# Kernel optimization log

Measured on AMD Instinct MI355X. Metric: run time of the kernel, lower is better.

The kernel has to match this reference:

```python
import jax, jax.numpy as jnp
import numpy as np

D_MODEL = 1024
D_STATE = 64
D_CONV = 4
EXPAND = 2
HEADDIM = 128
D_INNER = EXPAND * D_MODEL          # 2048
NHEADS = D_INNER // HEADDIM         # 16
CONV_DIM = D_INNER + 2 * D_STATE    # 2176 (ngroups=1)
D_IN_PROJ = 2 * D_INNER + 2 * D_STATE + NHEADS  # 4240
EPS = 1e-5


def _silu(x):
    return x * jax.nn.sigmoid(x)


def _causal_conv_silu(x, w, b):
    # x: [b, l, c]; w: [c, k] depthwise; b: [c]. Causal: pad left k-1, keep first L.
    L = x.shape[1]
    xp = jnp.pad(x, ((0, 0), (D_CONV - 1, 0), (0, 0)))
    out = b
    for k in range(D_CONV):  # tiny fixed kernel loop
        out = out + xp[:, k:k + L, :] * w[:, k]
    return _silu(out)


def _ssd_scan(x, dt, A, B, C):
    # x: [b,l,h,p], dt: [b,l,h], A: [h], B,C: [b,l,n] (ngroups=1, shared over heads)
    bsz = x.shape[0]

    def step(h, inp):
        x_t, dt_t, B_t, C_t = inp           # [b,h,p], [b,h], [b,n], [b,n]
        dA = jnp.exp(dt_t * A)              # [b,h]
        h = h * dA[:, :, None, None] + jnp.einsum('bh,bhp,bn->bhpn', dt_t, x_t, B_t)
        y = jnp.einsum('bhpn,bn->bhp', h, C_t)
        return h, y

    h0 = jnp.zeros((bsz, NHEADS, HEADDIM, D_STATE), x.dtype)
    xs = (jnp.moveaxis(x, 1, 0), jnp.moveaxis(dt, 1, 0),
          jnp.moveaxis(B, 1, 0), jnp.moveaxis(C, 1, 0))
    _, y = jax.lax.scan(step, h0, xs)       # y: [l,b,h,p]
    return jnp.moveaxis(y, 0, 1)


def _branch(zxbcdt, conv_w, conv_b, dt_bias, A_log, D, norm_w):
    # One direction of bimamba-v2: split, conv+silu, selective scan, D skip, gated RMSNorm.
    b, l, _ = zxbcdt.shape
    z = zxbcdt[..., :D_INNER]
    xBC = zxbcdt[..., D_INNER:D_INNER + CONV_DIM]
    dt = jax.nn.softplus(zxbcdt[..., -NHEADS:] + dt_bias)  # [b,l,h]
    A = -jnp.exp(A_log)                                     # [h]
    xBC = _causal_conv_silu(xBC, conv_w, conv_b)
    x = xBC[..., :D_INNER].reshape(b, l, NHEADS, HEADDIM)
    Bm = xBC[..., D_INNER:D_INNER + D_STATE]
    Cm = xBC[..., D_INNER + D_STATE:]
    y = _ssd_scan(x, dt, A, Bm, Cm) + D[None, None, :, None] * x
    y = y.reshape(b, l, D_INNER)
    # RMSNormGated, norm_before_gate=False: gate first, then normalize
    yz = y * _silu(z)
    return yz * jax.lax.rsqrt(jnp.mean(yz * yz, axis=-1, keepdims=True) + EPS) * norm_w


def setup_inputs() -> dict:
    key = jax.random.key(0)
    ks = jax.random.split(key, 12)
    B, L = 2, 4096

    def gauss(k, shape, scale):
        return jax.random.normal(k, shape, jnp.float32) * scale

    def dt_bias_init(k):
        lo, hi = np.log(0.001), np.log(0.1)
        dt = jnp.exp(jax.random.uniform(k, (NHEADS,)) * (hi - lo) + lo)
        dt = jnp.clip(dt, 1e-4, None)
        return dt + jnp.log(-jnp.expm1(-dt))  # softplus-inverse of dt

    return {
        'u': jax.random.normal(ks[0], (B, L, D_MODEL), jnp.float32),
        'in_proj_w': gauss(ks[1], (D_IN_PROJ, D_MODEL), 0.02),
        'conv_w': gauss(ks[2], (CONV_DIM, D_CONV), 0.2),
        'conv_b': jnp.zeros((CONV_DIM,), jnp.float32),
        'conv_w_bw': gauss(ks[3], (CONV_DIM, D_CONV), 0.2),
        'conv_b_bw': jnp.zeros((CONV_DIM,), jnp.float32),
        'dt_bias': dt_bias_init(ks[4]),
        'dt_bias_bw': dt_bias_init(ks[5]),
        'A_log': jnp.log(jax.random.uniform(ks[6], (NHEADS,), minval=1.0, maxval=16.0)),
        'A_b_log': jnp.log(jax.random.uniform(ks[7], (NHEADS,), minval=1.0, maxval=16.0)),
        'D': jnp.ones((NHEADS,), jnp.float32),
        'D_b': jnp.ones((NHEADS,), jnp.float32),
        'norm_w': jnp.ones((D_INNER,), jnp.float32),
        'out_proj_w': gauss(ks[8], (D_MODEL, D_INNER), 0.02),
    }


def reference(u, in_proj_w, conv_w, conv_b, conv_w_bw, conv_b_bw, dt_bias, dt_bias_bw,
              A_log, A_b_log, D, D_b, norm_w, out_proj_w):
    zxbcdt = u @ in_proj_w.T                                   # [b,l,4240]
    y_fw = _branch(zxbcdt, conv_w, conv_b, dt_bias, A_log, D, norm_w)
    y_bw = _branch(zxbcdt[:, ::-1, :], conv_w_bw, conv_b_bw, dt_bias_bw, A_b_log, D_b, norm_w)
    return (y_fw + y_bw[:, ::-1, :]) @ out_proj_w.T            # divide_out=False
```

## Files before the change

kernel.cpp:

```cpp
#include <hip/hip_runtime.h>
#include <hip/hip_bf16.h>
#include <math.h>

#define BB 2
#define LL 4096
#define DM 1024
#define DIP 4240
#define DIPP 4352
#define DI 2048
#define NH 16
#define HD 128
#define DS 64
#define CDIM 2176
#define MROWS (BB*LL)
#define Q 64
#define NC (LL/Q)
#define BH (BB*NH)
#define STR 72
#define CCH 16
#define NCHK (LL/CCH)

typedef __attribute__((ext_vector_type(8))) short bf16x8;
typedef __attribute__((ext_vector_type(4))) float f32x4;

__device__ __forceinline__ float silu_f(float x) { return x / (1.f + expf(-x)); }
__device__ __forceinline__ float softplus_f(float x) {
    return fmaxf(x, 0.f) + log1pf(expf(-fabsf(x)));
}
__device__ __forceinline__ float bf2f(unsigned short u) {
    return __uint_as_float(((unsigned int)u) << 16);
}
__device__ __forceinline__ unsigned short f2bf(float f) {
    unsigned int x = __float_as_uint(f);
    return (unsigned short)((x + 0x7fff + ((x >> 16) & 1)) >> 16);
}
__device__ __forceinline__ void gll16(const void* g, void* l) {
    __builtin_amdgcn_global_load_lds(
        (const __attribute__((address_space(1))) void*)g,
        (__attribute__((address_space(3))) void*)l,
        16, 0, 0);
}

__global__ __launch_bounds__(256)
void cvt_pad(const float* __restrict__ in, unsigned short* __restrict__ out,
             int rows_real, int rows_pad, int cols)
{
    int idx = blockIdx.x * 256 + threadIdx.x;
    int cols4 = cols >> 2;
    int total = rows_pad * cols4;
    if (idx >= total) return;
    int row = idx / cols4;
    int c4 = (idx - row * cols4) * 4;
    ushort4 o;
    if (row < rows_real) {
        float4 v = *reinterpret_cast<const float4*>(&in[(size_t)row * cols + c4]);
        o.x = f2bf(v.x); o.y = f2bf(v.y); o.z = f2bf(v.z); o.w = f2bf(v.w);
    } else {
        o = make_ushort4(0, 0, 0, 0);
    }
    *reinterpret_cast<ushort4*>(&out[(size_t)row * cols + c4]) = o;
}

__global__ __launch_bounds__(256)
void ucvt(const float* __restrict__ u, unsigned short* __restrict__ ub)
{
    int idx = blockIdx.x * 256 + threadIdx.x;
    const float* src = u + (size_t)idx * 8;
    float4 a = *reinterpret_cast<const float4*>(src);
    float4 b = *reinterpret_cast<const float4*>(src + 4);
    unsigned short o[8];
    o[0] = f2bf(a.x); o[1] = f2bf(a.y); o[2] = f2bf(a.z); o[3] = f2bf(a.w);
    o[4] = f2bf(b.x); o[5] = f2bf(b.y); o[6] = f2bf(b.z); o[7] = f2bf(b.w);
    *reinterpret_cast<uint4*>(&ub[(size_t)idx * 8]) = *reinterpret_cast<const uint4*>(o);
}

template<int OMODE>
__global__ __launch_bounds__(256)
void gemm_mfma(const unsigned short* __restrict__ Ap, int lda,
               const unsigned short* __restrict__ Bp, int K,
               void* __restrict__ Cp, int ldc, int Nreal)
{
    __shared__ alignas(16) unsigned short As[128 * 32];
    __shared__ alignas(16) unsigned short Bs[128 * 32];

    const int t = threadIdx.x;
    const int l = t & 63;
    const int bm = blockIdx.y * 128, bn = blockIdx.x * 128;
    const int wm = ((t >> 6) >> 1) * 64, wn = ((t >> 6) & 1) * 64;

    f32x4 acc[4][4];
    #pragma unroll
    for (int i = 0; i < 4; i++)
        #pragma unroll
        for (int j = 0; j < 4; j++)
            acc[i][j] = (f32x4){0.f, 0.f, 0.f, 0.f};

    for (int k0 = 0; k0 < K; k0 += 32) {
        #pragma unroll
        for (int i = 0; i < 2; i++) {
            int c = i * 256 + t;
            int row = c >> 2, ke = (c & 3) * 8;
            gll16(Ap + (size_t)(bm + row) * lda + k0 + ke, (char*)&As[0] + c * 16);
        }
        #pragma unroll
        for (int i = 0; i < 2; i++) {
            int c = i * 256 + t;
            int row = c >> 2, ke = (c & 3) * 8;
            gll16(Bp + (size_t)(bn + row) * K + k0 + ke, (char*)&Bs[0] + c * 16);
        }
        __syncthreads();

        bf16x8 af[4], bfr[4];
        #pragma unroll
        for (int mi = 0; mi < 4; mi++)
            af[mi] = *reinterpret_cast<const bf16x8*>(
                &As[(wm + mi * 16 + (l & 15)) * 32 + (l >> 4) * 8]);
        #pragma unroll
        for (int nj = 0; nj < 4; nj++)
            bfr[nj] = *reinterpret_cast<const bf16x8*>(
                &Bs[(wn + nj * 16 + (l & 15)) * 32 + (l >> 4) * 8]);
        #pragma unroll
        for (int mi = 0; mi < 4; mi++)
            #pragma unroll
            for (int nj = 0; nj < 4; nj++)
                acc[mi][nj] = __builtin_amdgcn_mfma_f32_16x16x32_bf16(
                    af[mi], bfr[nj], acc[mi][nj], 0, 0, 0);
        __syncthreads();
    }

    const int col_l = l & 15, rgrp = (l >> 4) * 4;
    #pragma unroll
    for (int mi = 0; mi < 4; mi++) {
        #pragma unroll
        for (int r = 0; r < 4; r++) {
            int gm = bm + wm + mi * 16 + rgrp + r;
            #pragma unroll
            for (int nj = 0; nj < 4; nj++) {
                int gn = bn + wn + nj * 16 + col_l;
                float v = acc[mi][nj][r];
                if (OMODE == 0) {
                    if (gn < Nreal)
                        ((unsigned short*)Cp)[(size_t)gm * ldc + gn] = f2bf(v);
                } else {
                    ((float*)Cp)[(size_t)gm * ldc + gn] = v;
                }
            }
        }
    }
}

__global__ __launch_bounds__(256)
void conv_fused(const unsigned short* __restrict__ zx,
                const float* __restrict__ cw0, const float* __restrict__ cb0,
                const float* __restrict__ cw1, const float* __restrict__ cb1,
                unsigned short* __restrict__ x0, unsigned short* __restrict__ x1)
{
    int idx = blockIdx.x * 256 + threadIdx.x;
    int c8 = idx % (CDIM / 8);
    int cg = idx / (CDIM / 8);
    int b  = cg >> 8;
    int ci = cg & (NCHK - 1);
    int c  = c8 * 8;
    int s0 = ci * CCH;

    float wt0[4][8], wt1[4][8], bv0[8], bv1[8];
    #pragma unroll
    for (int ch = 0; ch < 8; ch++) {
        float4 q0 = *reinterpret_cast<const float4*>(&cw0[(c + ch) * 4]);
        float4 q1 = *reinterpret_cast<const float4*>(&cw1[(c + ch) * 4]);
        wt0[0][ch] = q0.x; wt0[1][ch] = q0.y; wt0[2][ch] = q0.z; wt0[3][ch] = q0.w;
        wt1[0][ch] = q1.x; wt1[1][ch] = q1.y; wt1[2][ch] = q1.z; wt1[3][ch] = q1.w;
    }
    {
        float4 a0 = *reinterpret_cast<const float4*>(&cb0[c]);
        float4 a1 = *reinterpret_cast<const float4*>(&cb0[c + 4]);
        bv0[0]=a0.x; bv0[1]=a0.y; bv0[2]=a0.z; bv0[3]=a0.w;
        bv0[4]=a1.x; bv0[5]=a1.y; bv0[6]=a1.z; bv0[7]=a1.w;
        float4 d0 = *reinterpret_cast<const float4*>(&cb1[c]);
        float4 d1 = *reinterpret_cast<const float4*>(&cb1[c + 4]);
        bv1[0]=d0.x; bv1[1]=d0.y; bv1[2]=d0.z; bv1[3]=d0.w;
        bv1[4]=d1.x; bv1[5]=d1.y; bv1[6]=d1.z; bv1[7]=d1.w;
    }

    float win[4][8];

    #define LDROW(SL, S) do {                                                  \
        if ((S) >= 0) {                                                        \
            const unsigned short* _src = &zx[((size_t)b * LL + (S)) * DIP + DI + c]; \
            ushort4 _v0 = *reinterpret_cast<const ushort4*>(_src);             \
            ushort4 _v1 = *reinterpret_cast<const ushort4*>(_src + 4);         \
            win[SL][0] = bf2f(_v0.x); win[SL][1] = bf2f(_v0.y);                \
            win[SL][2] = bf2f(_v0.z); win[SL][3] = bf2f(_v0.w);                \
            win[SL][4] = bf2f(_v1.x); win[SL][5] = bf2f(_v1.y);                \
            win[SL][6] = bf2f(_v1.z); win[SL][7] = bf2f(_v1.w);                \
        } else {                                                               \
            _Pragma("unroll")                                                  \
            for (int _e = 0; _e < 8; _e++) win[SL][_e] = 0.f;                  \
        }                                                                      \
    } while (0)

    #define ZROW(SL) do {                                                      \
        _Pragma("unroll")                                                      \
        for (int _e = 0; _e < 8; _e++) win[SL][_e] = 0.f;                      \
    } while (0)

    #define EMIT0(PH, S) do {                                                  \
        float _a[8]; unsigned short _o[8];                                     \
        _Pragma("unroll")                                                      \
        for (int _ch = 0; _ch < 8; _ch++) {                                    \
            _a[_ch] = bv0[_ch];                                                \
            _a[_ch] = fmaf(wt0[0][_ch], win[((PH)+1)&3][_ch], _a[_ch]);        \
            _a[_ch] = fmaf(wt0[1][_ch], win[((PH)+2)&3][_ch], _a[_ch]);        \
            _a[_ch] = fmaf(wt0[2][_ch], win[((PH)+3)&3][_ch], _a[_ch]);        \
            _a[_ch] = fmaf(wt0[3][_ch], win[(PH)&3][_ch], _a[_ch]);            \
            _o[_ch] = f2bf(silu_f(_a[_ch]));                                   \
        }                                                                      \
        *reinterpret_cast<uint4*>(&x0[((size_t)b * LL + (S)) * CDIM + c]) =    \
            *reinterpret_cast<const uint4*>(_o);                               \
    } while (0)

    #define EMIT1(PH, S) do {                                                  \
        float _a[8]; unsigned short _o[8];                                     \
        _Pragma("unroll")                                                      \
        for (int _ch = 0; _ch < 8; _ch++) {                                    \
            _a[_ch] = bv1[_ch];                                                \
            _a[_ch] = fmaf(wt1[0][_ch], win[(PH)&3][_ch], _a[_ch]);            \
            _a[_ch] = fmaf(wt1[1][_ch], win[((PH)+3)&3][_ch], _a[_ch]);        \
            _a[_ch] = fmaf(wt1[2][_ch], win[((PH)+2)&3][_ch], _a[_ch]);        \
            _a[_ch] = fmaf(wt1[3][_ch], win[((PH)+1)&3][_ch], _a[_ch]);        \
            _o[_ch] = f2bf(silu_f(_a[_ch]));                                   \
        }                                                                      \
        *reinterpret_cast<uint4*>(&x1[((size_t)b * LL + (LL + 2 - (S))) * CDIM + c]) = \
            *reinterpret_cast<const uint4*>(_o);                               \
    } while (0)

    LDROW(1, s0 - 3);
    LDROW(2, s0 - 2);
    LDROW(3, s0 - 1);

    for (int it = 0; it < CCH; it += 4) {
        int sb = s0 + it;
        #pragma unroll
        for (int ph = 0; ph < 4; ph++) {
            int s = sb + ph;
            switch (ph) {
            case 0: LDROW(0, s); EMIT0(0, s); if (s >= 3) EMIT1(0, s); break;
            case 1: LDROW(1, s); EMIT0(1, s); if (s >= 3) EMIT1(1, s); break;
            case 2: LDROW(2, s); EMIT0(2, s); if (s >= 3) EMIT1(2, s); break;
            default: LDROW(3, s); EMIT0(3, s); if (s >= 3) EMIT1(3, s); break;
            }
        }
    }
    if (ci == NCHK - 1) {
        ZROW(0); EMIT1(0, LL);
        ZROW(1); EMIT1(1, LL + 1);
        ZROW(2); EMIT1(2, LL + 2);
    }
    #undef LDROW
    #undef ZROW
    #undef EMIT0
    #undef EMIT1
}

__global__ __launch_bounds__(256)
void ssd_state(const unsigned short* __restrict__ xc, const unsigned short* __restrict__ zx,
               const float* __restrict__ dtb, const float* __restrict__ A_log,
               unsigned short* __restrict__ hbuf, float* __restrict__ dtsum, int dir)
{
    int bh = blockIdx.x / NC;
    int c  = blockIdx.x % NC;
    int b = bh >> 4, h = bh & 15;
    float Ah = -expf(A_log[h]);
    float dtbh = dtb[h];
    int row0 = b * LL + c * Q;

    __shared__ alignas(16) unsigned short XT[128 * STR];
    __shared__ alignas(16) unsigned short wBT[64 * STR];
    __shared__ float dts_s[Q];
    __shared__ float cum_s[Q];

    const int tid = threadIdx.x;
    const int l = tid & 63;
    const int wid = tid >> 6;

    #pragma unroll
    for (int it = 0; it < 4; it++) {
        int idx = it * 256 + tid;
        int j = idx >> 4;
        int pblk = idx & 15;
        const unsigned short* src = &xc[(size_t)(row0 + j) * CDIM + h * HD + pblk * 8];
        ushort4 v0 = *reinterpret_cast<const ushort4*>(src);
        ushort4 v1 = *reinterpret_cast<const ushort4*>(src + 4);
        unsigned short xv[8] = {v0.x, v0.y, v0.z, v0.w, v1.x, v1.y, v1.z, v1.w};
        int jx = j ^ ((pblk & 7) << 3);
        #pragma unroll
        for (int e = 0; e < 8; e++)
            XT[(pblk * 8 + e) * STR + jx] = xv[e];
    }
    if (tid < Q) {
        int rr = c * Q + tid;
        int ls = dir ? (LL - 1 - rr) : rr;
        dts_s[tid] = softplus_f(bf2f(zx[(size_t)(b * LL + ls) * DIP + (DIP - NH) + h]) + dtbh);
    }
    __syncthreads();
    if (tid < Q) {
        float s = 0.f;
        for (int k = 0; k <= tid; k++) s += dts_s[k];
        cum_s[tid] = s;
    }
    __syncthreads();
    float cumlast = cum_s[Q - 1];
    if (tid == 0) dtsum[bh * NC + c] = cumlast;

    #pragma unroll
    for (int it = 0; it < 2; it++) {
        int idx = it * 256 + tid;
        int j = idx >> 3, n0 = (idx & 7) * 8;
        const unsigned short* src = &xc[(size_t)(row0 + j) * CDIM + DI + n0];
        ushort4 v0 = *reinterpret_cast<const ushort4*>(src);
        ushort4 v1 = *reinterpret_cast<const ushort4*>(src + 4);
        unsigned short bv[8] = {v0.x, v0.y, v0.z, v0.w, v1.x, v1.y, v1.z, v1.w};
        float wj = expf(Ah * (cumlast - cum_s[j])) * dts_s[j];
        #pragma unroll
        for (int e = 0; e < 8; e++)
            wBT[(n0 + e) * STR + j] = f2bf(wj * bf2f(bv[e]));
    }
    __syncthreads();

    f32x4 acc[2][4];
    #pragma unroll
    for (int i = 0; i < 2; i++)
        #pragma unroll
        for (int j = 0; j < 4; j++)
            acc[i][j] = (f32x4){0.f, 0.f, 0.f, 0.f};

    const int p0w = wid * 32;
    #pragma unroll
    for (int kk = 0; kk < 2; kk++) {
        bf16x8 af[2], bfr[4];
        #pragma unroll
        for (int mi = 0; mi < 2; mi++) {
            int p = p0w + mi * 16 + (l & 15);
            int col = (kk * 32 + (l >> 4) * 8) ^ (((p >> 3) & 7) << 3);
            af[mi] = *reinterpret_cast<const bf16x8*>(&XT[p * STR + col]);
        }
        #pragma unroll
        for (int nj = 0; nj < 4; nj++)
            bfr[nj] = *reinterpret_cast<const bf16x8*>(
                &wBT[(nj * 16 + (l & 15)) * STR + kk * 32 + (l >> 4) * 8]);
        #pragma unroll
        for (int mi = 0; mi < 2; mi++)
            #pragma unroll
            for (int nj = 0; nj < 4; nj++)
                acc[mi][nj] = __builtin_amdgcn_mfma_f32_16x16x32_bf16(
                    af[mi], bfr[nj], acc[mi][nj], 0, 0, 0);
    }

    size_t hb = ((size_t)c * BH + bh) * (HD * DS);
    #pragma unroll
    for (int mi = 0; mi < 2; mi++)
        #pragma unroll
        for (int r = 0; r < 4; r++) {
            int p = p0w + mi * 16 + (l >> 4) * 4 + r;
            #pragma unroll
            for (int nj = 0; nj < 4; nj++) {
                int n = nj * 16 + (l & 15);
                hbuf[hb + (size_t)p * DS + n] = f2bf(acc[mi][nj][r]);
            }
        }
}

__global__ __launch_bounds__(256)
void ssd_interchunk(unsigned short* __restrict__ hbuf, const float* __restrict__ dtsum,
                    const float* __restrict__ A_log)
{
    int bh  = blockIdx.x >> 5;
    int seg = blockIdx.x & 31;
    int h = bh & 15;
    float Ah = -expf(A_log[h]);
    int off = seg * 256 + threadIdx.x;
    float hst = 0.f;
    for (int c = 0; c < NC; c++) {
        size_t idx = ((size_t)c * BH + bh) * (HD * DS) + off;
        float s = bf2f(hbuf[idx]);
        hbuf[idx] = f2bf(hst);
        hst = fmaf(hst, expf(Ah * dtsum[bh * NC + c]), s);
    }
}

__global__ __launch_bounds__(256)
void ssd_intra(unsigned short* __restrict__ xc, const unsigned short* __restrict__ hbuf,
               const unsigned short* __restrict__ zx, const float* __restrict__ dtb,
               const float* __restrict__ A_log, const float* __restrict__ Dv, int dir)
{
    int bh = blockIdx.x / NC;
    int c  = blockIdx.x % NC;
    int b = bh >> 4, h = bh & 15;
    float Ah = -expf(A_log[h]);
    float Dh = Dv[h];
    float dtbh = dtb[h];
    int row0 = b * LL + c * Q;

    __shared__ alignas(16) unsigned short Cm[64 * STR];
    __shared__ alignas(16) unsigned short Bm[64 * STR];
    __shared__ alignas(16) unsigned short Mw[64 * STR];
    __shared__ alignas(16) unsigned short XT[128 * STR];
    __shared__ alignas(16) unsigned short hm[128 * STR];
    __shared__ float dts_s[Q];
    __shared__ float cum_s[Q];

    const int tid = threadIdx.x;
    const int l = tid & 63;
    const int wid = tid >> 6;

    #pragma unroll
    for (int it = 0; it < 4; it++) {
        int idx = it * 256 + tid;
        int j = idx >> 4;
        int pblk = idx & 15;
        const unsigned short* src = &xc[(size_t)(row0 + j) * CDIM + h * HD + pblk * 8];
        ushort4 v0 = *reinterpret_cast<const ushort4*>(src);
        ushort4 v1 = *reinterpret_cast<const ushort4*>(src + 4);
        unsigned short xv[8] = {v0.x, v0.y, v0.z, v0.w, v1.x, v1.y, v1.z, v1.w};
        int jx = j ^ ((pblk & 7) << 3);
        #pragma unroll
        for (int e = 0; e < 8; e++)
            XT[(pblk * 8 + e) * STR + jx] = xv[e];
    }
    #pragma unroll
    for (int it = 0; it < 2; it++) {
        int idx = it * 256 + tid;
        int j = idx >> 3, n0 = (idx & 7) * 8;
        *reinterpret_cast<uint4*>(&Bm[j * STR + n0]) =
            *reinterpret_cast<const uint4*>(&xc[(size_t)(row0 + j) * CDIM + DI + n0]);
        *reinterpret_cast<uint4*>(&Cm[j * STR + n0]) =
            *reinterpret_cast<const uint4*>(&xc[(size_t)(row0 + j) * CDIM + DI + DS + n0]);
    }
    {
        size_t hb = ((size_t)c * BH + bh) * (HD * DS);
        #pragma unroll
        for (int it = 0; it < 4; it++) {
            int idx = it * 256 + tid;
            int p = idx >> 3, n0 = (idx & 7) * 8;
            *reinterpret_cast<uint4*>(&hm[p * STR + n0]) =
                *reinterpret_cast<const uint4*>(&hbuf[hb + (size_t)p * DS + n0]);
        }
    }
    if (tid < Q) {
        int rr = c * Q + tid;
        int ls = dir ? (LL - 1 - rr) : rr;
        dts_s[tid] = softplus_f(bf2f(zx[(size_t)(b * LL + ls) * DIP + (DIP - NH) + h]) + dtbh);
    }
    __syncthreads();
    if (tid < Q) {
        float s = 0.f;
        for (int k = 0; k <= tid; k++) s += dts_s[k];
        cum_s[tid] = s;
    }
    __syncthreads();

    {
        const int i0 = (wid >> 1) * 32, j0 = (wid & 1) * 32;
        f32x4 g[2][2];
        #pragma unroll
        for (int i = 0; i < 2; i++)
            #pragma unroll
            for (int j = 0; j < 2; j++)
                g[i][j] = (f32x4){0.f, 0.f, 0.f, 0.f};
        #pragma unroll
        for (int kk = 0; kk < 2; kk++) {
            bf16x8 ca[2], bb[2];
            #pragma unroll
            for (int mi = 0; mi < 2; mi++)
                ca[mi] = *reinterpret_cast<const bf16x8*>(
                    &Cm[(i0 + mi * 16 + (l & 15)) * STR + kk * 32 + (l >> 4) * 8]);
            #pragma unroll
            for (int nj = 0; nj < 2; nj++)
                bb[nj] = *reinterpret_cast<const bf16x8*>(
                    &Bm[(j0 + nj * 16 + (l & 15)) * STR + kk * 32 + (l >> 4) * 8]);
            #pragma unroll
            for (int mi = 0; mi < 2; mi++)
                #pragma unroll
                for (int nj = 0; nj < 2; nj++)
                    g[mi][nj] = __builtin_amdgcn_mfma_f32_16x16x32_bf16(
                        ca[mi], bb[nj], g[mi][nj], 0, 0, 0);
        }
        #pragma unroll
        for (int mi = 0; mi < 2; mi++)
            #pragma unroll
            for (int nj = 0; nj < 2; nj++)
                #pragma unroll
                for (int r = 0; r < 4; r++) {
                    int i = i0 + mi * 16 + (l >> 4) * 4 + r;
                    int j = j0 + nj * 16 + (l & 15);
                    float wgt = 0.f;
                    if (j < i)       wgt = expf(Ah * (cum_s[i] - cum_s[j])) * dts_s[j];
                    else if (j == i) wgt = dts_s[j];
                    float mv = g[mi][nj][r] * wgt + (j == i ? Dh : 0.f);
                    Mw[i * STR + j] = f2bf(mv);
                }
    }
    __syncthreads();

    const int yi0 = (wid >> 1) * 32, yp0 = (wid & 1) * 64;
    f32x4 y1[2][4], y2[2][4];
    #pragma unroll
    for (int i = 0; i < 2; i++)
        #pragma unroll
        for (int j = 0; j < 4; j++) {
            y1[i][j] = (f32x4){0.f, 0.f, 0.f, 0.f};
            y2[i][j] = (f32x4){0.f, 0.f, 0.f, 0.f};
        }
    #pragma unroll
    for (int kk = 0; kk < 2; kk++) {
        bf16x8 ma[2], xb[4];
        #pragma unroll
        for (int mi = 0; mi < 2; mi++)
            ma[mi] = *reinterpret_cast<const bf16x8*>(
                &Mw[(yi0 + mi * 16 + (l & 15)) * STR + kk * 32 + (l >> 4) * 8]);
        #pragma unroll
        for (int nj = 0; nj < 4; nj++) {
            int p = yp0 + nj * 16 + (l & 15);
            int col = (kk * 32 + (l >> 4) * 8) ^ (((p >> 3) & 7) << 3);
            xb[nj] = *reinterpret_cast<const bf16x8*>(&XT[p * STR + col]);
        }
        #pragma unroll
        for (int mi = 0; mi < 2; mi++)
            #pragma unroll
            for (int nj = 0; nj < 4; nj++)
                y1[mi][nj] = __builtin_amdgcn_mfma_f32_16x16x32_bf16(
                    ma[mi], xb[nj], y1[mi][nj], 0, 0, 0);
    }
    #pragma unroll
    for (int kk = 0; kk < 2; kk++) {
        bf16x8 ca[2], hbf[4];
        #pragma unroll
        for (int mi = 0; mi < 2; mi++)
            ca[mi] = *reinterpret_cast<const bf16x8*>(
                &Cm[(yi0 + mi * 16 + (l & 15)) * STR + kk * 32 + (l >> 4) * 8]);
        #pragma unroll
        for (int nj = 0; nj < 4; nj++)
            hbf[nj] = *reinterpret_cast<const bf16x8*>(
                &hm[(yp0 + nj * 16 + (l & 15)) * STR + kk * 32 + (l >> 4) * 8]);
        #pragma unroll
        for (int mi = 0; mi < 2; mi++)
            #pragma unroll
            for (int nj = 0; nj < 4; nj++)
                y2[mi][nj] = __builtin_amdgcn_mfma_f32_16x16x32_bf16(
                    ca[mi], hbf[nj], y2[mi][nj], 0, 0, 0);
    }
    __syncthreads();

    unsigned short* Yl = &XT[0];
    #pragma unroll
    for (int mi = 0; mi < 2; mi++)
        #pragma unroll
        for (int r = 0; r < 4; r++) {
            int i = yi0 + mi * 16 + (l >> 4) * 4 + r;
            float Pi = expf(Ah * cum_s[i]);
            #pragma unroll
            for (int nj = 0; nj < 4; nj++) {
                int p = yp0 + nj * 16 + (l & 15);
                Yl[i * 136 + p] = f2bf(y1[mi][nj][r] + Pi * y2[mi][nj][r]);
            }
        }
    __syncthreads();
    #pragma unroll
    for (int it = 0; it < 4; it++) {
        int idx = it * 256 + tid;
        int i = idx >> 4, p0 = (idx & 15) * 8;
        *reinterpret_cast<uint4*>(&xc[(size_t)(row0 + i) * CDIM + h * HD + p0]) =
            *reinterpret_cast<const uint4*>(&Yl[i * 136 + p0]);
    }
}

__global__ __launch_bounds__(256)
void branch_final(const unsigned short* __restrict__ xcin, const unsigned short* __restrict__ zx,
                  const float* __restrict__ nw, unsigned short* __restrict__ xout, int dir)
{
    int row = blockIdx.x;
    int rr = row & (LL - 1);
    int b  = row >> 12;
    int l  = dir ? (LL - 1 - rr) : rr;

    const unsigned short* yrow = xcin + (size_t)row * CDIM;
    const unsigned short* zrow = zx + (size_t)(b * LL + l) * DIP;
    int c = threadIdx.x * 8;

    float v[8];
    float ss = 0.f;
    {
        ushort4 y0 = *reinterpret_cast<const ushort4*>(&yrow[c]);
        ushort4 y1 = *reinterpret_cast<const ushort4*>(&yrow[c + 4]);
        ushort4 z0 = *reinterpret_cast<const ushort4*>(&zrow[c]);
        ushort4 z1 = *reinterpret_cast<const ushort4*>(&zrow[c + 4]);
        unsigned short yv[8] = {y0.x, y0.y, y0.z, y0.w, y1.x, y1.y, y1.z, y1.w};
        unsigned short zv[8] = {z0.x, z0.y, z0.z, z0.w, z1.x, z1.y, z1.z, z1.w};
        #pragma unroll
        for (int ch = 0; ch < 8; ch++) {
            float val = bf2f(yv[ch]) * silu_f(bf2f(zv[ch]));
            v[ch] = val;
            ss = fmaf(val, val, ss);
        }
    }
    #pragma unroll
    for (int o = 32; o > 0; o >>= 1) ss += __shfl_down(ss, o);
    __shared__ float red[4];
    if ((threadIdx.x & 63) == 0) red[threadIdx.x >> 6] = ss;
    __syncthreads();
    ss = red[0] + red[1] + red[2] + red[3];
    float scale = rsqrtf(ss * (1.f / DI) + 1e-5f);

    float w[8];
    {
        float4 w0 = *reinterpret_cast<const float4*>(&nw[c]);
        float4 w1 = *reinterpret_cast<const float4*>(&nw[c + 4]);
        w[0] = w0.x; w[1] = w0.y; w[2] = w0.z; w[3] = w0.w;
        w[4] = w1.x; w[5] = w1.y; w[6] = w1.z; w[7] = w1.w;
    }

    unsigned short* orow = xout + (size_t)(b * LL + l) * CDIM;
    unsigned short o[8];
    if (dir) {
        ushort4 p0 = *reinterpret_cast<const ushort4*>(&orow[c]);
        ushort4 p1 = *reinterpret_cast<const ushort4*>(&orow[c + 4]);
        unsigned short pv[8] = {p0.x, p0.y, p0.z, p0.w, p1.x, p1.y, p1.z, p1.w};
        #pragma unroll
        for (int ch = 0; ch < 8; ch++)
            o[ch] = f2bf(bf2f(pv[ch]) + v[ch] * scale * w[ch]);
    } else {
        #pragma unroll
        for (int ch = 0; ch < 8; ch++)
            o[ch] = f2bf(v[ch] * scale * w[ch]);
    }
    *reinterpret_cast<uint4*>(&orow[c]) = *reinterpret_cast<const uint4*>(o);
}

extern "C" void kernel_launch(void* const* d_in, const int* in_sizes, int n_in,
                              void* d_out, int out_size, void* d_ws, size_t ws_size,
                              hipStream_t stream)
{
    const float* u       = (const float*)d_in[0];
    const float* w_in    = (const float*)d_in[1];
    const float* conv_w  = (const float*)d_in[2];
    const float* conv_b  = (const float*)d_in[3];
    const float* conv_wb = (const float*)d_in[4];
    const float* conv_bb = (const float*)d_in[5];
    const float* dt_bias  = (const float*)d_in[6];
    const float* dt_biasb = (const float*)d_in[7];
    const float* A_log   = (const float*)d_in[8];
    const float* A_b_log = (const float*)d_in[9];
    const float* Dp      = (const float*)d_in[10];
    const float* D_b     = (const float*)d_in[11];
    const float* norm_w  = (const float*)d_in[12];
    const float* w_out   = (const float*)d_in[13];
    float* out = (float*)d_out;

    unsigned short* zx    = (unsigned short*)d_ws;
    unsigned short* xc    = zx + (size_t)MROWS * DIP;
    unsigned short* xc2   = xc + (size_t)MROWS * CDIM;
    unsigned short* hb_ub = xc2 + (size_t)MROWS * CDIM;
    unsigned short* wbin  = hb_ub + (size_t)NC * BH * HD * DS;
    unsigned short* wbout = wbin + (size_t)DIPP * DM;
    float* dtsum = (float*)(wbout + (size_t)DM * DI);

    unsigned short* ub   = hb_ub;
    unsigned short* hbuf = hb_ub;

    cvt_pad<<<(DIPP * (DM / 4) + 255) / 256, 256, 0, stream>>>(w_in, wbin, DIP, DIPP, DM);
    cvt_pad<<<(DM * (DI / 4) + 255) / 256, 256, 0, stream>>>(w_out, wbout, DM, DM, DI);
    ucvt<<<(MROWS * DM / 8) / 256, 256, 0, stream>>>(u, ub);

    {
        dim3 grid(DIPP / 128, MROWS / 128);
        gemm_mfma<0><<<grid, 256, 0, stream>>>(ub, DM, wbin, DM, zx, DIP, DIP);
    }

    conv_fused<<<(CDIM / 8) * BB * NCHK / 256, 256, 0, stream>>>(
        zx, conv_w, conv_b, conv_wb, conv_bb, xc, xc2);

    for (int dir = 0; dir < 2; dir++) {
        const float* dtb = dir ? dt_biasb : dt_bias;
        const float* Al  = dir ? A_b_log  : A_log;
        const float* Dd  = dir ? D_b      : Dp;
        unsigned short* xb = dir ? xc2 : xc;

        ssd_state<<<BH * NC, 256, 0, stream>>>(xb, zx, dtb, Al, hbuf, dtsum, dir);
        ssd_interchunk<<<BH * 32, 256, 0, stream>>>(hbuf, dtsum, Al);
        ssd_intra<<<BH * NC, 256, 0, stream>>>(xb, hbuf, zx, dtb, Al, Dd, dir);
        branch_final<<<MROWS, 256, 0, stream>>>(xb, zx, norm_w, xc, dir);
    }

    {
        dim3 grid(DM / 128, MROWS / 128);
        gemm_mfma<1><<<grid, 256, 0, stream>>>(xc, CDIM, wbout, DI, out, DM, DM);
    }
}
```

Baseline: 513.3 us.

## Fuse both branch finals, swizzle GEMM tiles, shuffle-scan cumsum, coalesce state stores

```diff
diff --git a/kernel.cpp b/kernel.cpp
--- a/kernel.cpp
+++ b/kernel.cpp
@@ -85,7 +85,13 @@
 
     const int t = threadIdx.x;
     const int l = t & 63;
-    const int bm = blockIdx.y * 128, bn = blockIdx.x * 128;
+
+    int lin = blockIdx.y * gridDim.x + blockIdx.x;
+    int nwg = gridDim.x * gridDim.y;
+    int swz = (lin & 7) * (nwg >> 3) + (lin >> 3);
+    int bxs = swz % gridDim.x, bys = swz / gridDim.x;
+
+    const int bm = bys * 128, bn = bxs * 128;
     const int wm = ((t >> 6) >> 1) * 64, wn = ((t >> 6) & 1) * 64;
 
     f32x4 acc[4][4];
@@ -300,13 +306,15 @@
     if (tid < Q) {
         int rr = c * Q + tid;
         int ls = dir ? (LL - 1 - rr) : rr;
-        dts_s[tid] = softplus_f(bf2f(zx[(size_t)(b * LL + ls) * DIP + (DIP - NH) + h]) + dtbh);
-    }
-    __syncthreads();
-    if (tid < Q) {
-        float s = 0.f;
-        for (int k = 0; k <= tid; k++) s += dts_s[k];
-        cum_s[tid] = s;
+        float dtv = softplus_f(bf2f(zx[(size_t)(b * LL + ls) * DIP + (DIP - NH) + h]) + dtbh);
+        float ps = dtv;
+        #pragma unroll
+        for (int o = 1; o < 64; o <<= 1) {
+            float t2 = __shfl_up(ps, o);
+            if (tid >= o) ps += t2;
+        }
+        dts_s[tid] = dtv;
+        cum_s[tid] = ps;
     }
     __syncthreads();
     float cumlast = cum_s[Q - 1];
@@ -356,7 +364,8 @@
                     af[mi], bfr[nj], acc[mi][nj], 0, 0, 0);
     }
 
-    size_t hb = ((size_t)c * BH + bh) * (HD * DS);
+    __syncthreads();
+    unsigned short* Sl = &XT[0];
     #pragma unroll
     for (int mi = 0; mi < 2; mi++)
         #pragma unroll
@@ -365,9 +374,18 @@
             #pragma unroll
             for (int nj = 0; nj < 4; nj++) {
                 int n = nj * 16 + (l & 15);
-                hbuf[hb + (size_t)p * DS + n] = f2bf(acc[mi][nj][r]);
+                Sl[p * STR + n] = f2bf(acc[mi][nj][r]);
             }
         }
+    __syncthreads();
+    size_t hb = ((size_t)c * BH + bh) * (HD * DS);
+    #pragma unroll
+    for (int it = 0; it < 4; it++) {
+        int idx = it * 256 + tid;
+        int p = idx >> 3, n0 = (idx & 7) * 8;
+        *reinterpret_cast<uint4*>(&hbuf[hb + (size_t)p * DS + n0]) =
+            *reinterpret_cast<const uint4*>(&Sl[p * STR + n0]);
+    }
 }
 
 __global__ __launch_bounds__(256)
@@ -449,13 +467,15 @@
     if (tid < Q) {
         int rr = c * Q + tid;
         int ls = dir ? (LL - 1 - rr) : rr;
-        dts_s[tid] = softplus_f(bf2f(zx[(size_t)(b * LL + ls) * DIP + (DIP - NH) + h]) + dtbh);
-    }
-    __syncthreads();
-    if (tid < Q) {
-        float s = 0.f;
-        for (int k = 0; k <= tid; k++) s += dts_s[k];
-        cum_s[tid] = s;
+        float dtv = softplus_f(bf2f(zx[(size_t)(b * LL + ls) * DIP + (DIP - NH) + h]) + dtbh);
+        float ps = dtv;
+        #pragma unroll
+        for (int o = 1; o < 64; o <<= 1) {
+            float t2 = __shfl_up(ps, o);
+            if (tid >= o) ps += t2;
+        }
+        dts_s[tid] = dtv;
+        cum_s[tid] = ps;
     }
     __syncthreads();
 
@@ -575,41 +595,55 @@
 }
 
 __global__ __launch_bounds__(256)
-void branch_final(const unsigned short* __restrict__ xcin, const unsigned short* __restrict__ zx,
-                  const float* __restrict__ nw, unsigned short* __restrict__ xout, int dir)
+void branch_final2(unsigned short* __restrict__ xc_fw, const unsigned short* __restrict__ xc_bw,
+                   const unsigned short* __restrict__ zx, const float* __restrict__ nw)
 {
     int row = blockIdx.x;
-    int rr = row & (LL - 1);
+    int ll = row & (LL - 1);
     int b  = row >> 12;
-    int l  = dir ? (LL - 1 - rr) : rr;
-
-    const unsigned short* yrow = xcin + (size_t)row * CDIM;
-    const unsigned short* zrow = zx + (size_t)(b * LL + l) * DIP;
+
+    unsigned short* yfw = xc_fw + (size_t)row * CDIM;
+    const unsigned short* ybw = xc_bw + ((size_t)b * LL + (LL - 1 - ll)) * CDIM;
+    const unsigned short* zrow = zx + (size_t)row * DIP;
     int c = threadIdx.x * 8;
 
-    float v[8];
-    float ss = 0.f;
+    float vf[8], vb[8];
+    float sf = 0.f, sb = 0.f;
     {
-        ushort4 y0 = *reinterpret_cast<const ushort4*>(&yrow[c]);
-        ushort4 y1 = *reinterpret_cast<const ushort4*>(&yrow[c + 4]);
+        ushort4 f0 = *reinterpret_cast<const ushort4*>(&yfw[c]);
+        ushort4 f1 = *reinterpret_cast<const ushort4*>(&yfw[c + 4]);
+        ushort4 w0 = *reinterpret_cast<const ushort4*>(&ybw[c]);
+        ushort4 w1 = *reinterpret_cast<const ushort4*>(&ybw[c + 4]);
         ushort4 z0 = *reinterpret_cast<const ushort4*>(&zrow[c]);
         ushort4 z1 = *reinterpret_cast<const ushort4*>(&zrow[c + 4]);
-        unsigned short yv[8] = {y0.x, y0.y, y0.z, y0.w, y1.x, y1.y, y1.z, y1.w};
+        unsigned short fv[8] = {f0.x, f0.y, f0.z, f0.w, f1.x, f1.y, f1.z, f1.w};
+        unsigned short wv[8] = {w0.x, w0.y, w0.z, w0.w, w1.x, w1.y, w1.z, w1.w};
         unsigned short zv[8] = {z0.x, z0.y, z0.z, z0.w, z1.x, z1.y, z1.z, z1.w};
         #pragma unroll
         for (int ch = 0; ch < 8; ch++) {
-            float val = bf2f(yv[ch]) * silu_f(bf2f(zv[ch]));
-            v[ch] = val;
-            ss = fmaf(val, val, ss);
-        }
-    }
-    #pragma unroll
-    for (int o = 32; o > 0; o >>= 1) ss += __shfl_down(ss, o);
-    __shared__ float red[4];
-    if ((threadIdx.x & 63) == 0) red[threadIdx.x >> 6] = ss;
-    __syncthreads();
-    ss = red[0] + red[1] + red[2] + red[3];
-    float scale = rsqrtf(ss * (1.f / DI) + 1e-5f);
+            float g = silu_f(bf2f(zv[ch]));
+            float a = bf2f(fv[ch]) * g;
+            float d = bf2f(wv[ch]) * g;
+            vf[ch] = a; vb[ch] = d;
+            sf = fmaf(a, a, sf);
+            sb = fmaf(d, d, sb);
+        }
+    }
+    #pragma unroll
+    for (int o = 32; o > 0; o >>= 1) {
+        sf += __shfl_down(sf, o);
+        sb += __shfl_down(sb, o);
+    }
+    __shared__ float redf[4], redb[4];
+    if ((threadIdx.x & 63) == 0) {
+        redf[threadIdx.x >> 6] = sf;
+        redb[threadIdx.x >> 6] = sb;
+    }
+    __syncthreads();
+    sf = redf[0] + redf[1] + redf[2] + redf[3];
+    sb = redb[0] + redb[1] + redb[2] + redb[3];
+    float scf = rsqrtf(sf * (1.f / DI) + 1e-5f);
+    float scb = rsqrtf(sb * (1.f / DI) + 1e-5f);
 
     float w[8];
     {
@@ -618,22 +652,11 @@
         w[0] = w0.x; w[1] = w0.y; w[2] = w0.z; w[3] = w0.w;
         w[4] = w1.x; w[5] = w1.y; w[6] = w1.z; w[7] = w1.w;
     }
-
-    unsigned short* orow = xout + (size_t)(b * LL + l) * CDIM;
     unsigned short o[8];
-    if (dir) {
-        ushort4 p0 = *reinterpret_cast<const ushort4*>(&orow[c]);
-        ushort4 p1 = *reinterpret_cast<const ushort4*>(&orow[c + 4]);
-        unsigned short pv[8] = {p0.x, p0.y, p0.z, p0.w, p1.x, p1.y, p1.z, p1.w};
-        #pragma unroll
-        for (int ch = 0; ch < 8; ch++)
-            o[ch] = f2bf(bf2f(pv[ch]) + v[ch] * scale * w[ch]);
-    } else {
-        #pragma unroll
-        for (int ch = 0; ch < 8; ch++)
-            o[ch] = f2bf(v[ch] * scale * w[ch]);
-    }
-    *reinterpret_cast<uint4*>(&orow[c]) = *reinterpret_cast<const uint4*>(o);
+    #pragma unroll
+    for (int ch = 0; ch < 8; ch++)
+        o[ch] = f2bf((vf[ch] * scf + vb[ch] * scb) * w[ch]);
+    *reinterpret_cast<uint4*>(&yfw[c]) = *reinterpret_cast<const uint4*>(o);
 }
 
 extern "C" void kernel_launch(void* const* d_in, const int* in_sizes, int n_in,
@@ -688,8 +711,8 @@
         ssd_state<<<BH * NC, 256, 0, stream>>>(xb, zx, dtb, Al, hbuf, dtsum, dir);
         ssd_interchunk<<<BH * 32, 256, 0, stream>>>(hbuf, dtsum, Al);
         ssd_intra<<<BH * NC, 256, 0, stream>>>(xb, hbuf, zx, dtb, Al, Dd, dir);
-        branch_final<<<MROWS, 256, 0, stream>>>(xb, zx, norm_w, xc, dir);
-    }
+    }
+    branch_final2<<<MROWS, 256, 0, stream>>>(xc, xc2, zx, norm_w);
 
     {
         dim3 grid(DM / 128, MROWS / 128);
```

After: 487.1 us. 1.05x faster.
